# Optimization experiments

Measured on AMD Instinct MI355X. Metric: run time of the kernel, lower is better.

The kernel has to match this reference:

```python
import jax, jax.numpy as jnp
import numpy as np


def setup_inputs() -> dict:
    key = jax.random.key(0)
    k1, k2 = jax.random.split(key)
    N_ACTIVE = 262144
    C = 64            # nPlanes
    S = 64            # spatial_size per dim (3D)
    B = 8             # batch size
    features = jax.random.normal(k1, (N_ACTIVE, C), dtype=jnp.float32)
    # rule book: flat linear index of each active site into (b, z, y, x)
    idx = jax.random.randint(k2, (N_ACTIVE,), 0, B * S * S * S, dtype=jnp.int64)
    return {"features": features, "idx": idx, "spatial_size": S, "batch_size": B}


def reference(features, idx, spatial_size, batch_size):
    # Scatter sparse active-site features into dense grid.
    # features: [N, C], idx: [N] flat index over (b, z, y, x).
    N, C = features.shape
    S = spatial_size
    B = batch_size
    dense = jnp.zeros((B * S * S * S, C), dtype=features.dtype)
    # active sites in SparseConvNet are unique -> add == set, but add has a
    # well-defined gradient (pure gather) matching SparseToDense_updateGradInput
    dense = dense.at[idx].add(features)
    # [B, S, S, S, C] -> [B, C, S, S, S] (torch channels-first layout)
    dense = dense.reshape(B, S, S, S, C)
    return jnp.transpose(dense, (0, 4, 1, 2, 3))
```

## Files before the change

kernel.cpp:

```cpp
#include <hip/hip_runtime.h>


#define C_CH      64
#define LOG_C     6
#define LOG_S3    18
#define S3        (1 << LOG_S3)
#define NCELL     (8 * S3)
#define OUT_ELEMS (8LL * C_CH * S3)

__global__ void init_head_kernel(int* __restrict__ head) {
    int i = blockIdx.x * blockDim.x + threadIdx.x;
    ((int4*)head)[i] = make_int4(-1, -1, -1, -1);
}

__global__ void build_lists_kernel(const int* __restrict__ idx,
                                   int* __restrict__ head,
                                   int* __restrict__ nxt, int n) {
    int i = blockIdx.x * blockDim.x + threadIdx.x;
    if (i < n) {
        int cell = idx[i];
        nxt[i] = atomicExch(&head[cell], i);
    }
}

__global__ void emit_kernel(const float* __restrict__ feat,
                            const int* __restrict__ head,
                            const int* __restrict__ nxt,
                            float* __restrict__ out) {
    long long t  = (long long)blockIdx.x * blockDim.x + threadIdx.x;
    long long o4 = t << 2;
    int s4 = (int)(o4 & (S3 - 1));
    int bc = (int)(o4 >> LOG_S3);
    int c  = bc & (C_CH - 1);
    int b  = bc >> LOG_C;

    const int4 h4 = *(const int4*)(head + ((long long)b << LOG_S3) + s4);

    float4 v;
    int p; float acc;
    p = h4.x; acc = 0.f;
    while (p >= 0) { acc += feat[((long long)p << LOG_C) + c]; p = nxt[p]; }
    v.x = acc;
    p = h4.y; acc = 0.f;
    while (p >= 0) { acc += feat[((long long)p << LOG_C) + c]; p = nxt[p]; }
    v.y = acc;
    p = h4.z; acc = 0.f;
    while (p >= 0) { acc += feat[((long long)p << LOG_C) + c]; p = nxt[p]; }
    v.z = acc;
    p = h4.w; acc = 0.f;
    while (p >= 0) { acc += feat[((long long)p << LOG_C) + c]; p = nxt[p]; }
    v.w = acc;

    *(float4*)(out + o4) = v;
}

__global__ void zero_out_kernel(float4* __restrict__ out) {
    long long i = (long long)blockIdx.x * blockDim.x + threadIdx.x;
    out[i] = make_float4(0.f, 0.f, 0.f, 0.f);
}

__global__ void scatter_atomic_kernel(const float* __restrict__ feat,
                                      const int* __restrict__ idx,
                                      float* __restrict__ out, int n) {
    int i = blockIdx.x * blockDim.x + threadIdx.x;
    int nn = i >> LOG_C;
    int c  = i & (C_CH - 1);
    if (nn < n) {
        int cell = idx[nn];
        int b = cell >> LOG_S3;
        int s = cell & (S3 - 1);
        long long o = (((long long)((b << LOG_C) + c)) << LOG_S3) + s;
        atomicAdd(&out[o], feat[i]);
    }
}

extern "C" void kernel_launch(void* const* d_in, const int* in_sizes, int n_in,
                              void* d_out, int out_size, void* d_ws, size_t ws_size,
                              hipStream_t stream) {
    const float* feat = (const float*)d_in[0];
    const int*   idx  = (const int*)d_in[1];
    float*       out  = (float*)d_out;
    const int N = in_sizes[1];

    const size_t head_bytes = (size_t)NCELL * sizeof(int);
    const size_t next_bytes = (size_t)N * sizeof(int);

    if (ws_size >= head_bytes + next_bytes) {
        int* head = (int*)d_ws;
        int* nxt  = (int*)((char*)d_ws + head_bytes);

        {
            int threads = NCELL / 4;
            init_head_kernel<<<threads / 256, 256, 0, stream>>>(head);
        }
        build_lists_kernel<<<(N + 255) / 256, 256, 0, stream>>>(idx, head, nxt, N);
        {
            long long threads = OUT_ELEMS / 4;
            emit_kernel<<<(int)(threads / 256), 256, 0, stream>>>(feat, head, nxt, out);
        }
    } else {
        zero_out_kernel<<<(int)(OUT_ELEMS / 4 / 256), 256, 0, stream>>>((float4*)out);
        scatter_atomic_kernel<<<(N * C_CH) / 256, 256, 0, stream>>>(feat, idx, out, N);
    }
}
```

Before: 695.3 us.

## Emit dense output via per-site LDS tile transpose with vectorized feature reads

Replaces the per-output-element emit kernel, which walked the linked list once per channel with strided scalar feature loads, with a tiled kernel. Each thread owns one spatial site and reads contiguous float4 chunks of its feature rows into a 16-channel shared-memory tile. The tile is then written out channel-major with coalesced float4 nontemporal stores. This cuts redundant list traversal and uncoalesced gathers, at the cost of shared-memory staging, extra barriers and lower occupancy per block.

```diff
diff --git a/kernel.cpp b/kernel.cpp
--- a/kernel.cpp
+++ b/kernel.cpp
@@ -7,6 +7,8 @@
 #define S3        (1 << LOG_S3)
 #define NCELL     (8 * S3)
 #define OUT_ELEMS (8LL * C_CH * S3)
+#define TILE_S    256
+#define CHUNK_C   16
 
 __global__ void init_head_kernel(int* __restrict__ head) {
     int i = blockIdx.x * blockDim.x + threadIdx.x;
@@ -23,35 +25,62 @@
     }
 }
 
-__global__ void emit_kernel(const float* __restrict__ feat,
-                            const int* __restrict__ head,
-                            const int* __restrict__ nxt,
-                            float* __restrict__ out) {
-    long long t  = (long long)blockIdx.x * blockDim.x + threadIdx.x;
-    long long o4 = t << 2;
-    int s4 = (int)(o4 & (S3 - 1));
-    int bc = (int)(o4 >> LOG_S3);
-    int c  = bc & (C_CH - 1);
-    int b  = bc >> LOG_C;
+__global__ void __launch_bounds__(256, 2)
+emit_tile_kernel(const float* __restrict__ feat,
+                 const int* __restrict__ head,
+                 const int* __restrict__ nxt,
+                 float* __restrict__ out) {
+    __shared__ float tile[CHUNK_C * TILE_S];
 
-    const int4 h4 = *(const int4*)(head + ((long long)b << LOG_S3) + s4);
+    const int b      = blockIdx.x >> 10;
+    const int s_base = (blockIdx.x & 1023) << 8;
+    const int t      = threadIdx.x;
 
-    float4 v;
-    int p; float acc;
-    p = h4.x; acc = 0.f;
-    while (p >= 0) { acc += feat[((long long)p << LOG_C) + c]; p = nxt[p]; }
-    v.x = acc;
-    p = h4.y; acc = 0.f;
-    while (p >= 0) { acc += feat[((long long)p << LOG_C) + c]; p = nxt[p]; }
-    v.y = acc;
-    p = h4.z; acc = 0.f;
-    while (p >= 0) { acc += feat[((long long)p << LOG_C) + c]; p = nxt[p]; }
-    v.z = acc;
-    p = h4.w; acc = 0.f;
-    while (p >= 0) { acc += feat[((long long)p << LOG_C) + c]; p = nxt[p]; }
-    v.w = acc;
+    const int h = head[((long long)b << LOG_S3) + s_base + t];
 
-    *(float4*)(out + o4) = v;
+    const int lane = t & 63;
+    const int wave = t >> 6;
+
+    #pragma unroll
+    for (int chunk = 0; chunk < C_CH / CHUNK_C; ++chunk) {
+        float4* t4 = (float4*)tile;
+        #pragma unroll
+        for (int k = 0; k < 4; ++k)
+            t4[t + 256 * k] = make_float4(0.f, 0.f, 0.f, 0.f);
+        __syncthreads();
+
+        int p = h;
+        while (p >= 0) {
+            const float4* fr = (const float4*)(feat + ((long long)p << LOG_C)
+                                               + (chunk << 4));
+            float4 f0 = fr[0], f1 = fr[1], f2 = fr[2], f3 = fr[3];
+            float* col = tile + t;
+            col[0*TILE_S]  += f0.x;  col[1*TILE_S]  += f0.y;
+            col[2*TILE_S]  += f0.z;  col[3*TILE_S]  += f0.w;
+            col[4*TILE_S]  += f1.x;  col[5*TILE_S]  += f1.y;
+            col[6*TILE_S]  += f1.z;  col[7*TILE_S]  += f1.w;
+            col[8*TILE_S]  += f2.x;  col[9*TILE_S]  += f2.y;
+            col[10*TILE_S] += f2.z;  col[11*TILE_S] += f2.w;
+            col[12*TILE_S] += f3.x;  col[13*TILE_S] += f3.y;
+            col[14*TILE_S] += f3.z;  col[15*TILE_S] += f3.w;
+            p = nxt[p];
+        }
+        __syncthreads();
+
+        #pragma unroll
+        for (int r = 0; r < 4; ++r) {
+            const int c = wave + (r << 2);
+            float4 v = *(float4*)(tile + c * TILE_S + (lane << 2));
+            const int c_glob = (b << LOG_C) + (chunk << 4) + c;
+            float4* dst = (float4*)(out + (((long long)c_glob) << LOG_S3)
+                                    + s_base + (lane << 2));
+            __builtin_nontemporal_store(v.x, &dst->x);
+            __builtin_nontemporal_store(v.y, &dst->y);
+            __builtin_nontemporal_store(v.z, &dst->z);
+            __builtin_nontemporal_store(v.w, &dst->w);
+        }
+        __syncthreads();
+    }
 }
 
 __global__ void zero_out_kernel(float4* __restrict__ out) {
@@ -89,15 +118,9 @@
         int* head = (int*)d_ws;
         int* nxt  = (int*)((char*)d_ws + head_bytes);
 
-        {
-            int threads = NCELL / 4;
-            init_head_kernel<<<threads / 256, 256, 0, stream>>>(head);
-        }
+        init_head_kernel<<<NCELL / 4 / 256, 256, 0, stream>>>(head);
         build_lists_kernel<<<(N + 255) / 256, 256, 0, stream>>>(idx, head, nxt, N);
-        {
-            long long threads = OUT_ELEMS / 4;
-            emit_kernel<<<(int)(threads / 256), 256, 0, stream>>>(feat, head, nxt, out);
-        }
+        emit_tile_kernel<<<NCELL / TILE_S, 256, 0, stream>>>(feat, head, nxt, out);
     } else {
         zero_out_kernel<<<(int)(OUT_ELEMS / 4 / 256), 256, 0, stream>>>((float4*)out);
         scatter_atomic_kernel<<<(N * C_CH) / 256, 256, 0, stream>>>(feat, idx, out, N);
```

Result: faster. 614.6 us (-11.6%).

## Emit all channels per thread with register accumulators and vector feature loads

Applied to the files above, without the earlier changes.

Restructures the emit kernel so each thread owns four cells and loops over channels in four 16-channel chunks. It walks each linked list once per chunk, reading features as 16-byte vectors, and accumulates into a 64-entry register array. Output is written with nontemporal float4 stores. This cuts the head loads and list walks that were repeated 64 times per cell, at the cost of far fewer threads (2048 blocks) and high register pressure that lowers occupancy.

```diff
diff --git a/kernel.cpp b/kernel.cpp
--- a/kernel.cpp
+++ b/kernel.cpp
@@ -7,6 +7,8 @@
 #define S3        (1 << LOG_S3)
 #define NCELL     (8 * S3)
 #define OUT_ELEMS (8LL * C_CH * S3)
+
+typedef float v4f __attribute__((ext_vector_type(4)));
 
 __global__ void init_head_kernel(int* __restrict__ head) {
     int i = blockIdx.x * blockDim.x + threadIdx.x;
@@ -23,35 +25,49 @@
     }
 }
 
-__global__ void emit_kernel(const float* __restrict__ feat,
-                            const int* __restrict__ head,
-                            const int* __restrict__ nxt,
-                            float* __restrict__ out) {
-    long long t  = (long long)blockIdx.x * blockDim.x + threadIdx.x;
-    long long o4 = t << 2;
-    int s4 = (int)(o4 & (S3 - 1));
-    int bc = (int)(o4 >> LOG_S3);
-    int c  = bc & (C_CH - 1);
-    int b  = bc >> LOG_C;
+__global__ void __launch_bounds__(256)
+emit_reg_kernel(const float* __restrict__ feat,
+                const int* __restrict__ head,
+                const int* __restrict__ nxt,
+                float* __restrict__ out) {
+    const int b      = blockIdx.x >> 8;
+    const int s_base = (blockIdx.x & 255) << 10;
+    const int cell0  = s_base + (threadIdx.x << 2);
 
-    const int4 h4 = *(const int4*)(head + ((long long)b << LOG_S3) + s4);
+    const int4 h4 = *(const int4*)(head + ((size_t)b << LOG_S3) + cell0);
+    int hs[4] = {h4.x, h4.y, h4.z, h4.w};
 
-    float4 v;
-    int p; float acc;
-    p = h4.x; acc = 0.f;
-    while (p >= 0) { acc += feat[((long long)p << LOG_C) + c]; p = nxt[p]; }
-    v.x = acc;
-    p = h4.y; acc = 0.f;
-    while (p >= 0) { acc += feat[((long long)p << LOG_C) + c]; p = nxt[p]; }
-    v.y = acc;
-    p = h4.z; acc = 0.f;
-    while (p >= 0) { acc += feat[((long long)p << LOG_C) + c]; p = nxt[p]; }
-    v.z = acc;
-    p = h4.w; acc = 0.f;
-    while (p >= 0) { acc += feat[((long long)p << LOG_C) + c]; p = nxt[p]; }
-    v.w = acc;
+    #pragma unroll 1
+    for (int chunk = 0; chunk < 4; ++chunk) {
+        float acc[64];
+        #pragma unroll
+        for (int i = 0; i < 64; ++i) acc[i] = 0.f;
 
-    *(float4*)(out + o4) = v;
+        #pragma unroll
+        for (int j = 0; j < 4; ++j) {
+            int p = hs[j];
+            while (p >= 0) {
+                const v4f* fr = (const v4f*)(feat + ((size_t)p << LOG_C)
+                                             + (chunk << 4));
+                v4f f0 = fr[0], f1 = fr[1], f2 = fr[2], f3 = fr[3];
+                float* a = acc + j * 16;
+                a[0]  += f0.x; a[1]  += f0.y; a[2]  += f0.z; a[3]  += f0.w;
+                a[4]  += f1.x; a[5]  += f1.y; a[6]  += f1.z; a[7]  += f1.w;
+                a[8]  += f2.x; a[9]  += f2.y; a[10] += f2.z; a[11] += f2.w;
+                a[12] += f3.x; a[13] += f3.y; a[14] += f3.z; a[15] += f3.w;
+                p = nxt[p];
+            }
+        }
+
+        const size_t obase = ((size_t)((b << LOG_C) + (chunk << 4)) << LOG_S3)
+                             + cell0;
+        #pragma unroll
+        for (int cc = 0; cc < 16; ++cc) {
+            v4f v = {acc[cc], acc[16 + cc], acc[32 + cc], acc[48 + cc]};
+            __builtin_nontemporal_store(
+                v, (v4f*)(out + obase + ((size_t)cc << LOG_S3)));
+        }
+    }
 }
 
 __global__ void zero_out_kernel(float4* __restrict__ out) {
@@ -89,15 +105,9 @@
         int* head = (int*)d_ws;
         int* nxt  = (int*)((char*)d_ws + head_bytes);
 
-        {
-            int threads = NCELL / 4;
-            init_head_kernel<<<threads / 256, 256, 0, stream>>>(head);
-        }
+        init_head_kernel<<<NCELL / 4 / 256, 256, 0, stream>>>(head);
         build_lists_kernel<<<(N + 255) / 256, 256, 0, stream>>>(idx, head, nxt, N);
-        {
-            long long threads = OUT_ELEMS / 4;
-            emit_kernel<<<(int)(threads / 256), 256, 0, stream>>>(feat, head, nxt, out);
-        }
+        emit_reg_kernel<<<NCELL / 1024, 256, 0, stream>>>(feat, head, nxt, out);
     } else {
         zero_out_kernel<<<(int)(OUT_ELEMS / 4 / 256), 256, 0, stream>>>((float4*)out);
         scatter_atomic_kernel<<<(N * C_CH) / 256, 256, 0, stream>>>(feat, idx, out, N);
```

After: 624.3 us. -10.2%, faster.
